# Performance work log

Hardware: AMD Instinct MI355X
Metric: run time of the kernel (lower is better)

## Reference

```python
import jax, jax.numpy as jnp
import numpy as np

D_MODEL = 1024
NUM_HEADS = 16
D_K = D_MODEL // NUM_HEADS


def setup_inputs() -> dict:
    key = jax.random.key(0)
    k_x, k_q, k_k, k_v, k_o = jax.random.split(key, 5)
    s = 1.0 / np.sqrt(D_MODEL)
    return {
        "x": jax.random.normal(k_x, (2, 2048, D_MODEL), dtype=jnp.float32),
        "W_q": jax.random.normal(k_q, (D_MODEL, D_MODEL), dtype=jnp.float32) * s,
        "W_k": jax.random.normal(k_k, (D_MODEL, D_MODEL), dtype=jnp.float32) * s,
        "W_v": jax.random.normal(k_v, (D_MODEL, D_MODEL), dtype=jnp.float32) * s,
        "W_o": jax.random.normal(k_o, (D_MODEL, D_MODEL), dtype=jnp.float32) * s,
    }


def reference(x, W_q, W_k, W_v, W_o):
    B, S, D = x.shape
    H, dk = NUM_HEADS, D_K
    # nn.Linear(y) = y @ W.T ; weights stored as (out, in)
    def proj(W):
        return (x @ W.T).reshape(B, S, H, dk).transpose(0, 2, 1, 3)  # (B,H,S,dk)
    Q, K, V = proj(W_q), proj(W_k), proj(W_v)
    scores = jnp.einsum("bhqd,bhkd->bhqk", Q, K) / np.sqrt(dk)  # (B,H,S,S)
    attn = jax.nn.softmax(scores, axis=-1)
    out = jnp.einsum("bhqk,bhkd->bhqd", attn, V)  # (B,H,S,dk)
    out = out.transpose(0, 2, 1, 3).reshape(B, S, D)
    return out @ W_o.T
```

## Files before the change

### kernel.cpp

```cpp
#include <hip/hip_runtime.h>
#include <hip/hip_bf16.h>

#define SEQ 2048
#define DM  1024
#define NH  16
#define DK  64
#define MROWS 4096

typedef __attribute__((ext_vector_type(8))) short short8;
typedef __attribute__((ext_vector_type(4))) short short4v;
typedef __attribute__((ext_vector_type(4))) float float4v;
typedef __attribute__((ext_vector_type(2))) unsigned uint2v;

typedef const __attribute__((address_space(1))) unsigned gu32;
typedef __attribute__((address_space(3))) unsigned lu32;

__device__ __forceinline__ void gl2lds16(const void* g, void* l) {
  __builtin_amdgcn_global_load_lds((gu32*)g, (lu32*)l, 16, 0, 0);
}

__device__ __forceinline__ short f2bf(float f) {
  union { float f; unsigned u; } v; v.f = f;
  unsigned r = v.u + 0x7fffu + ((v.u >> 16) & 1u);
  return (short)(r >> 16);
}

#if __has_builtin(__builtin_amdgcn_exp2f)
#define EXP2(x) __builtin_amdgcn_exp2f(x)
#else
#define EXP2(x) exp2f(x)
#endif

__device__ __forceinline__ unsigned pack_bfu(float a, float b) {
  unsigned ua = __float_as_uint(a) + 0x8000u;
  unsigned ub = __float_as_uint(b) + 0x8000u;
#if __has_builtin(__builtin_amdgcn_perm)
  return __builtin_amdgcn_perm(ub, ua, 0x07060302u);
#else
  return (ua >> 16) | (ub & 0xffff0000u);
#endif
}

__global__ __launch_bounds__(256) void cvt_kernel(
    const float* __restrict__ in, short* __restrict__ out) {
  int i = blockIdx.x * 256 + threadIdx.x;
  float4v f = ((const float4v*)in)[i];
  short4v s;
#pragma unroll
  for (int j = 0; j < 4; ++j) s[j] = f2bf(f[j]);
  ((short4v*)out)[i] = s;
}

__global__ __launch_bounds__(256) void cvt4_kernel(
    const float* __restrict__ a, const float* __restrict__ b,
    const float* __restrict__ c, const float* __restrict__ d,
    short* __restrict__ out) {
  const float* srcs[4] = {a, b, c, d};
  const float* s = srcs[blockIdx.y];
  int i = blockIdx.x * 256 + threadIdx.x;
  float4v f = ((const float4v*)s)[i];
  short4v sv;
#pragma unroll
  for (int j = 0; j < 4; ++j) sv[j] = f2bf(f[j]);
  ((short4v*)(out + (size_t)blockIdx.y * DM * DM))[i] = sv;
}

template<int WMW, int WNW, int WNSZ, typename TC>
__global__ __launch_bounds__(WMW*WNW*64, 3) void gemm_bt(
    const short* __restrict__ A, const short* __restrict__ Bw0,
    TC* __restrict__ C0, int M, int N, int K, size_t strB, size_t strC,
    short* __restrict__ vtOut, float qs0)
{
  constexpr int WAVES = WMW * WNW, THREADS = WAVES * 64;
  constexpr int TM = WMW * 64, TN = WNW * WNSZ, NI = WNSZ / 16;
  constexpr int CA = TM * 64 / (8 * THREADS);
  constexpr int CB = TN * 64 / (8 * THREADS);
  constexpr int SM_SZ = (WMW == 2 && WNW == 2) ? 128 * 136 : (TM + TN) * 64;
  __shared__ __align__(16) short SMEM[SM_SZ];
  short* Al = SMEM;
  short* Bl = SMEM + TM * 64;

  const short* Bw = Bw0 + (size_t)blockIdx.z * strB;
  TC* C = C0 + (size_t)blockIdx.z * strC;

  const int tid  = threadIdx.x;
  const int lane = tid & 63, wave = tid >> 6;
  const int l16  = lane & 15, quad = lane >> 4;
  const int wm   = (wave / WNW) * 64, wn = (wave % WNW) * WNSZ;
  const int cm   = blockIdx.y * TM, cn = blockIdx.x * TN;

  float4v acc[4][NI];
#pragma unroll
  for (int i = 0; i < 4; ++i)
#pragma unroll
    for (int j = 0; j < NI; ++j)
#pragma unroll
      for (int r = 0; r < 4; ++r) acc[i][j][r] = 0.f;

  const short* ag = A  + (size_t)cm * K;
  const short* bg = Bw + (size_t)cn * K;

  auto stage = [&](int k0) {
#pragma unroll
    for (int i = 0; i < CA; ++i) {
      int c = i * THREADS + tid;
      int row = c >> 3, cg = (c & 7) ^ (row & 7);
      gl2lds16(ag + (size_t)row * K + k0 + cg * 8,
               &Al[(i * WAVES + wave) * 512]);
    }
#pragma unroll
    for (int i = 0; i < CB; ++i) {
      int c = i * THREADS + tid;
      int row = c >> 3, cg = (c & 7) ^ (row & 7);
      gl2lds16(bg + (size_t)row * K + k0 + cg * 8,
               &Bl[(i * WAVES + wave) * 512]);
    }
  };
  auto compute = [&]() {
#pragma unroll
    for (int ks = 0; ks < 2; ++ks) {
      const int sw = ((ks * 4 + quad) ^ (l16 & 7)) << 3;
      short8 af[4], bfr[NI];
#pragma unroll
      for (int mi = 0; mi < 4; ++mi)
        af[mi] = *(const short8*)&Al[(wm + mi*16 + l16) * 64 + sw];
#pragma unroll
      for (int ni = 0; ni < NI; ++ni)
        bfr[ni] = *(const short8*)&Bl[(wn + ni*16 + l16) * 64 + sw];
#pragma unroll
      for (int mi = 0; mi < 4; ++mi)
#pragma unroll
        for (int ni = 0; ni < NI; ++ni)
          acc[mi][ni] = __builtin_amdgcn_mfma_f32_16x16x32_bf16(
              af[mi], bfr[ni], acc[mi][ni], 0, 0, 0);
    }
  };

  for (int k0 = 0; k0 < K; k0 += 64) {
    stage(k0);
    __syncthreads();
    compute();
    __syncthreads();
  }

  const float scl = (blockIdx.z == 0) ? qs0 : 1.f;

  if constexpr (WMW == 2 && WNW == 2) {
    if (vtOut != nullptr && blockIdx.z == 2) {
      short* T = SMEM;
#pragma unroll
      for (int mi = 0; mi < 4; ++mi)
#pragma unroll
        for (int ni = 0; ni < 4; ++ni)
#pragma unroll
          for (int r = 0; r < 4; ++r)
            T[(wn + ni*16 + l16) * 136 + wm + mi*16 + quad*4 + r] =
                f2bf(acc[mi][ni][r]);
      __syncthreads();
      const int nrow = tid >> 1, mo = (tid & 1) * 64;
      const int b = cm >> 11;
      const int s0 = (cm & (SEQ - 1)) + mo;
      short* vt = vtOut + ((size_t)b * DM + cn + nrow) * SEQ + s0;
#pragma unroll
      for (int j = 0; j < 8; ++j)
        *(short8*)(vt + j * 8) = *(const short8*)&T[nrow * 136 + mo + j * 8];
      return;
    }
  }
#pragma unroll
  for (int mi = 0; mi < 4; ++mi)
#pragma unroll
    for (int ni = 0; ni < NI; ++ni)
#pragma unroll
      for (int r = 0; r < 4; ++r) {
        int m = cm + wm + mi*16 + quad*4 + r;
        int n = cn + wn + ni*16 + l16;
        float v = acc[mi][ni][r] * scl;
        if constexpr (sizeof(TC) == 2) C[(size_t)m * N + n] = f2bf(v);
        else                           C[(size_t)m * N + n] = v;
      }
}

__global__ __launch_bounds__(256, 3) void flash_kernel(
    const short* __restrict__ Q, const short* __restrict__ Kg,
    const short* __restrict__ VTg, short* __restrict__ AO)
{
  __shared__ __align__(16) short Kl[2][64 * 64];
  __shared__ __align__(16) short Vt[2][64 * 64];
  __shared__ __align__(16) short Pl[4][32 * 64];
  __shared__ float lsumL[4][32];
  const int tid  = threadIdx.x;
  const int lane = tid & 63, wave = tid >> 6;
  const int l16  = lane & 15, quad = lane >> 4;
  const int hc   = blockIdx.x * DK;
  const int q0   = blockIdx.y * 128;
  const size_t base = (size_t)blockIdx.z * SEQ;

  short8 qfr[2][2];
#pragma unroll
  for (int qf = 0; qf < 2; ++qf)
#pragma unroll
    for (int ks = 0; ks < 2; ++ks)
      qfr[qf][ks] = *(const short8*)(Q + (base + q0 + wave*32 + qf*16 + l16) * DM
                                     + hc + ks*32 + quad*8);

  float4v O[2][4];
  float lsum[2] = {0.f, 0.f};
#pragma unroll
  for (int mt = 0; mt < 2; ++mt)
#pragma unroll
    for (int nt = 0; nt < 4; ++nt)
#pragma unroll
      for (int r = 0; r < 4; ++r) O[mt][nt][r] = 0.f;

  const float4v z4 = {0.f, 0.f, 0.f, 0.f};
  const short* vtb = VTg + ((size_t)blockIdx.z * DM + hc) * SEQ;

  auto stageKV = [&](int buf, int kb) {
#pragma unroll
    for (int i = 0; i < 2; ++i) {
      int c = i * 256 + tid;
      int row = c >> 3, cg = (c & 7) ^ (row & 7);
      gl2lds16(Kg + (base + kb*64 + row) * DM + hc + cg * 8,
               &Kl[buf][(i * 4 + wave) * 512]);
      gl2lds16(vtb + (size_t)row * SEQ + kb*64 + cg * 8,
               &Vt[buf][(i * 4 + wave) * 512]);
    }
  };

  stageKV(0, 0);
  __syncthreads();

  int cur = 0;
  for (int kb = 0; kb < SEQ / 64; ++kb) {
    bool nxt = (kb + 1 < SEQ / 64);
    if (nxt) stageKV(cur ^ 1, kb + 1);

    float4v s[4][2];
#pragma unroll
    for (int kf = 0; kf < 4; ++kf) {
      const int rowb = (kf*16 + l16) * 64;
      short8 k0 = *(const short8*)&Kl[cur][rowb + ((quad       ^ (l16 & 7)) << 3)];
      short8 k1 = *(const short8*)&Kl[cur][rowb + (((4 + quad) ^ (l16 & 7)) << 3)];
#pragma unroll
      for (int qf = 0; qf < 2; ++qf) {
        float4v t = __builtin_amdgcn_mfma_f32_16x16x32_bf16(k0, qfr[qf][0], z4, 0, 0, 0);
        s[kf][qf]  = __builtin_amdgcn_mfma_f32_16x16x32_bf16(k1, qfr[qf][1], t, 0, 0, 0);
      }
    }
#pragma unroll
    for (int kf = 0; kf < 4; ++kf)
#pragma unroll
      for (int qf = 0; qf < 2; ++qf) {
        float p0 = EXP2(s[kf][qf][0]), p1 = EXP2(s[kf][qf][1]);
        float p2 = EXP2(s[kf][qf][2]), p3 = EXP2(s[kf][qf][3]);
        lsum[qf] += (p0 + p1) + (p2 + p3);
        uint2v pk;
        pk[0] = pack_bfu(p0, p1);
        pk[1] = pack_bfu(p2, p3);
        *(uint2v*)&Pl[wave][(qf*16 + l16) * 64 +
                            ((kf*16 + quad*4) ^ ((l16 & 7) << 3))] = pk;
      }
#pragma unroll
    for (int ks = 0; ks < 2; ++ks) {
      const int sw = ((ks*4 + quad) ^ (l16 & 7)) << 3;
      short8 pf[2];
#pragma unroll
      for (int mt = 0; mt < 2; ++mt)
        pf[mt] = *(const short8*)&Pl[wave][(mt*16 + l16) * 64 + sw];
#pragma unroll
      for (int nt = 0; nt < 4; ++nt) {
        short8 vf = *(const short8*)&Vt[cur][(nt*16 + l16) * 64 + sw];
#pragma unroll
        for (int mt = 0; mt < 2; ++mt)
          O[mt][nt] = __builtin_amdgcn_mfma_f32_16x16x32_bf16(
              pf[mt], vf, O[mt][nt], 0, 0, 0);
      }
    }
    __syncthreads();
    cur ^= 1;
  }

#pragma unroll
  for (int qf = 0; qf < 2; ++qf) {
    float l = lsum[qf];
    l += __shfl_xor(l, 16, 64);
    l += __shfl_xor(l, 32, 64);
    lsumL[wave][qf*16 + l16] = l;
  }
#pragma unroll
  for (int mt = 0; mt < 2; ++mt) {
    float inv[4];
#pragma unroll
    for (int r = 0; r < 4; ++r)
      inv[r] = 1.f / lsumL[wave][mt*16 + quad*4 + r];
#pragma unroll
    for (int nt = 0; nt < 4; ++nt)
#pragma unroll
      for (int r = 0; r < 4; ++r) {
        int m = q0 + wave*32 + mt*16 + quad*4 + r;
        AO[(base + m) * DM + hc + nt*16 + l16] = f2bf(O[mt][nt][r] * inv[r]);
      }
  }
}

extern "C" void kernel_launch(void* const* d_in, const int* in_sizes, int n_in,
                              void* d_out, int out_size, void* d_ws, size_t ws_size,
                              hipStream_t stream) {
  (void)in_sizes; (void)n_in; (void)out_size; (void)ws_size;
  const float* x  = (const float*)d_in[0];
  const float* Wq = (const float*)d_in[1];
  const float* Wk = (const float*)d_in[2];
  const float* Wv = (const float*)d_in[3];
  const float* Wo = (const float*)d_in[4];
  float* out = (float*)d_out;

  const size_t NX = (size_t)MROWS * DM;
  const size_t NW = (size_t)DM * DM;
  short* xb  = (short*)d_ws;
  short* Wqb = xb  + NX;
  short* Qb  = Wqb + 4 * NW;
  short* Kb  = Qb  + NX;
  short* AO  = Kb  + NX;
  short* VTb = AO  + NX;

  cvt_kernel<<<dim3(NX / 4 / 256), 256, 0, stream>>>(x, xb);
  cvt4_kernel<<<dim3(NW / 4 / 256, 4), 256, 0, stream>>>(Wq, Wk, Wv, Wo, Wqb);

  const float qs = 0.18033688011112042f;

  gemm_bt<2, 2, 64, short><<<dim3(DM / 128, MROWS / 128, 3), 256, 0, stream>>>(
      xb, Wqb, Qb, MROWS, DM, DM, NW, NX, VTb, qs);

  flash_kernel<<<dim3(NH, SEQ / 128, 2), 256, 0, stream>>>(Qb, Kb, VTb, AO);

  gemm_bt<1, 4, 32, float><<<dim3(DM / 128, MROWS / 64, 1), 256, 0, stream>>>(
      AO, Wqb + 3 * NW, out, MROWS, DM, DM, 0, 0, nullptr, 1.f);
}
```

Measured before the change: 181.8 us.

## Double-buffer GEMM LDS staging with BK=32 and a single barrier per step

The bf16 GEMM's K loop now uses BK=32 with two LDS buffers. The next slice is prefetched through global_load_lds while MFMAs run on the current one, and each step needs one barrier instead of two. The LDS swizzle is reworked for 32-wide rows, and the output GEMM's min-waves launch bound is lowered to 2. This aims to hide global load latency at the cost of more loop iterations, with fewer MFMAs per barrier.

```diff
diff --git a/kernel.cpp b/kernel.cpp
--- a/kernel.cpp
+++ b/kernel.cpp
@@ -65,20 +65,20 @@
   ((short4v*)(out + (size_t)blockIdx.y * DM * DM))[i] = sv;
 }
 
-template<int WMW, int WNW, int WNSZ, typename TC>
-__global__ __launch_bounds__(WMW*WNW*64, 3) void gemm_bt(
+template<int WMW, int WNW, int WNSZ, int MINW, typename TC>
+__global__ __launch_bounds__(WMW*WNW*64, MINW) void gemm_bt(
     const short* __restrict__ A, const short* __restrict__ Bw0,
     TC* __restrict__ C0, int M, int N, int K, size_t strB, size_t strC,
     short* __restrict__ vtOut, float qs0)
 {
   constexpr int WAVES = WMW * WNW, THREADS = WAVES * 64;
   constexpr int TM = WMW * 64, TN = WNW * WNSZ, NI = WNSZ / 16;
-  constexpr int CA = TM * 64 / (8 * THREADS);
-  constexpr int CB = TN * 64 / (8 * THREADS);
-  constexpr int SM_SZ = (WMW == 2 && WNW == 2) ? 128 * 136 : (TM + TN) * 64;
+  constexpr int CA = TM * 32 / (8 * THREADS);
+  constexpr int CB = TN * 32 / (8 * THREADS);
+  constexpr int STG = 2 * (TM + TN) * 32;
+  constexpr int SM_SZ = (WMW == 2 && WNW == 2) ?
+      (STG > 128 * 136 ? STG : 128 * 136) : STG;
   __shared__ __align__(16) short SMEM[SM_SZ];
-  short* Al = SMEM;
-  short* Bl = SMEM + TM * 64;
 
   const short* Bw = Bw0 + (size_t)blockIdx.z * strB;
   TC* C = C0 + (size_t)blockIdx.z * strC;
@@ -100,47 +100,52 @@
   const short* ag = A  + (size_t)cm * K;
   const short* bg = Bw + (size_t)cn * K;
 
-  auto stage = [&](int k0) {
+  auto stage = [&](int buf, int k0) {
 #pragma unroll
     for (int i = 0; i < CA; ++i) {
-      int c = i * THREADS + tid;
-      int row = c >> 3, cg = (c & 7) ^ (row & 7);
-      gl2lds16(ag + (size_t)row * K + k0 + cg * 8,
-               &Al[(i * WAVES + wave) * 512]);
+      int s = i * THREADS + tid;
+      int row = s >> 2, cgl = (s & 3) ^ ((row >> 1) & 3);
+      gl2lds16(ag + (size_t)row * K + k0 + cgl * 8,
+               &SMEM[buf * TM * 32 + (i * WAVES + wave) * 512]);
     }
 #pragma unroll
     for (int i = 0; i < CB; ++i) {
-      int c = i * THREADS + tid;
-      int row = c >> 3, cg = (c & 7) ^ (row & 7);
-      gl2lds16(bg + (size_t)row * K + k0 + cg * 8,
-               &Bl[(i * WAVES + wave) * 512]);
+      int s = i * THREADS + tid;
+      int row = s >> 2, cgl = (s & 3) ^ ((row >> 1) & 3);
+      gl2lds16(bg + (size_t)row * K + k0 + cgl * 8,
+               &SMEM[2 * TM * 32 + buf * TN * 32 + (i * WAVES + wave) * 512]);
     }
   };
-  auto compute = [&]() {
-#pragma unroll
-    for (int ks = 0; ks < 2; ++ks) {
-      const int sw = ((ks * 4 + quad) ^ (l16 & 7)) << 3;
-      short8 af[4], bfr[NI];
-#pragma unroll
-      for (int mi = 0; mi < 4; ++mi)
-        af[mi] = *(const short8*)&Al[(wm + mi*16 + l16) * 64 + sw];
+  auto compute = [&](int buf) {
+    const short* Al = &SMEM[buf * TM * 32];
+    const short* Bl = &SMEM[2 * TM * 32 + buf * TN * 32];
+    short8 af[4], bfr[NI];
+#pragma unroll
+    for (int mi = 0; mi < 4; ++mi) {
+      int row = wm + mi*16 + l16;
+      af[mi] = *(const short8*)&Al[row * 32 + ((quad ^ ((row >> 1) & 3)) << 3)];
+    }
+#pragma unroll
+    for (int ni = 0; ni < NI; ++ni) {
+      int row = wn + ni*16 + l16;
+      bfr[ni] = *(const short8*)&Bl[row * 32 + ((quad ^ ((row >> 1) & 3)) << 3)];
+    }
+#pragma unroll
+    for (int mi = 0; mi < 4; ++mi)
 #pragma unroll
       for (int ni = 0; ni < NI; ++ni)
-        bfr[ni] = *(const short8*)&Bl[(wn + ni*16 + l16) * 64 + sw];
-#pragma unroll
-      for (int mi = 0; mi < 4; ++mi)
-#pragma unroll
-        for (int ni = 0; ni < NI; ++ni)
-          acc[mi][ni] = __builtin_amdgcn_mfma_f32_16x16x32_bf16(
-              af[mi], bfr[ni], acc[mi][ni], 0, 0, 0);
-    }
+        acc[mi][ni] = __builtin_amdgcn_mfma_f32_16x16x32_bf16(
+            af[mi], bfr[ni], acc[mi][ni], 0, 0, 0);
   };
 
-  for (int k0 = 0; k0 < K; k0 += 64) {
-    stage(k0);
+  stage(0, 0);
+  __syncthreads();
+  int cur = 0;
+  for (int k0 = 0; k0 < K; k0 += 32) {
+    if (k0 + 32 < K) stage(cur ^ 1, k0 + 32);
+    compute(cur);
     __syncthreads();
-    compute();
-    __syncthreads();
+    cur ^= 1;
   }
 
   const float scl = (blockIdx.z == 0) ? qs0 : 1.f;
@@ -329,11 +334,11 @@
 
   const float qs = 0.18033688011112042f;
 
-  gemm_bt<2, 2, 64, short><<<dim3(DM / 128, MROWS / 128, 3), 256, 0, stream>>>(
+  gemm_bt<2, 2, 64, 3, short><<<dim3(DM / 128, MROWS / 128, 3), 256, 0, stream>>>(
       xb, Wqb, Qb, MROWS, DM, DM, NW, NX, VTb, qs);
 
   flash_kernel<<<dim3(NH, SEQ / 128, 2), 256, 0, stream>>>(Qb, Kb, VTb, AO);
 
-  gemm_bt<1, 4, 32, float><<<dim3(DM / 128, MROWS / 64, 1), 256, 0, stream>>>(
+  gemm_bt<1, 4, 32, 2, float><<<dim3(DM / 128, MROWS / 64, 1), 256, 0, stream>>>(
       AO, Wqb + 3 * NW, out, MROWS, DM, DM, 0, 0, nullptr, 1.f);
 }
```

After: 186.8 us. 2.8% more time.

## Shrink GEMM tiles and double flash waves per block for higher occupancy

Applied to the files above, without the earlier changes.

The GEMM kernel is re-templated on tile sizes: QKV projection uses 64x128 tiles and output projection 64x64 tiles, each with 2x2 waves holding 32-row fragments, with min-blocks raised to 6. The flash attention kernel now uses 8 waves of 16 query rows each instead of 4 waves of 32 rows, so each thread stages one K/V chunk and keeps fewer accumulators. The intent is to cut register pressure and launch more waves to hide latency. In exchange each tile gets less reuse per LDS load, and more global traffic is spent re-fetching A and B tiles.

```diff
diff --git a/kernel.cpp b/kernel.cpp
--- a/kernel.cpp
+++ b/kernel.cpp
@@ -65,17 +65,18 @@
   ((short4v*)(out + (size_t)blockIdx.y * DM * DM))[i] = sv;
 }
 
-template<int WMW, int WNW, int WNSZ, typename TC>
-__global__ __launch_bounds__(WMW*WNW*64, 3) void gemm_bt(
+template<int TM, int TN, int MINW, typename TC>
+__global__ __launch_bounds__(256, MINW) void gemm_bt(
     const short* __restrict__ A, const short* __restrict__ Bw0,
     TC* __restrict__ C0, int M, int N, int K, size_t strB, size_t strC,
     short* __restrict__ vtOut, float qs0)
 {
-  constexpr int WAVES = WMW * WNW, THREADS = WAVES * 64;
-  constexpr int TM = WMW * 64, TN = WNW * WNSZ, NI = WNSZ / 16;
-  constexpr int CA = TM * 64 / (8 * THREADS);
-  constexpr int CB = TN * 64 / (8 * THREADS);
-  constexpr int SM_SZ = (WMW == 2 && WNW == 2) ? 128 * 136 : (TM + TN) * 64;
+  constexpr int NI = TN / 32;
+  constexpr int CA = TM * 64 / (8 * 256);
+  constexpr int CB = TN * 64 / (8 * 256);
+  constexpr int STG = (TM + TN) * 64;
+  constexpr int TSZ = TN * 72;
+  constexpr int SM_SZ = (TN == 128 && TSZ > STG) ? TSZ : STG;
   __shared__ __align__(16) short SMEM[SM_SZ];
   short* Al = SMEM;
   short* Bl = SMEM + TM * 64;
@@ -86,12 +87,12 @@
   const int tid  = threadIdx.x;
   const int lane = tid & 63, wave = tid >> 6;
   const int l16  = lane & 15, quad = lane >> 4;
-  const int wm   = (wave / WNW) * 64, wn = (wave % WNW) * WNSZ;
+  const int wm   = (wave >> 1) * 32, wn = (wave & 1) * (TN / 2);
   const int cm   = blockIdx.y * TM, cn = blockIdx.x * TN;
 
-  float4v acc[4][NI];
-#pragma unroll
-  for (int i = 0; i < 4; ++i)
+  float4v acc[2][NI];
+#pragma unroll
+  for (int i = 0; i < 2; ++i)
 #pragma unroll
     for (int j = 0; j < NI; ++j)
 #pragma unroll
@@ -103,32 +104,30 @@
   auto stage = [&](int k0) {
 #pragma unroll
     for (int i = 0; i < CA; ++i) {
-      int c = i * THREADS + tid;
+      int c = i * 256 + tid;
       int row = c >> 3, cg = (c & 7) ^ (row & 7);
-      gl2lds16(ag + (size_t)row * K + k0 + cg * 8,
-               &Al[(i * WAVES + wave) * 512]);
+      gl2lds16(ag + (size_t)row * K + k0 + cg * 8, &Al[(i * 4 + wave) * 512]);
     }
 #pragma unroll
     for (int i = 0; i < CB; ++i) {
-      int c = i * THREADS + tid;
+      int c = i * 256 + tid;
       int row = c >> 3, cg = (c & 7) ^ (row & 7);
-      gl2lds16(bg + (size_t)row * K + k0 + cg * 8,
-               &Bl[(i * WAVES + wave) * 512]);
+      gl2lds16(bg + (size_t)row * K + k0 + cg * 8, &Bl[(i * 4 + wave) * 512]);
     }
   };
   auto compute = [&]() {
 #pragma unroll
     for (int ks = 0; ks < 2; ++ks) {
       const int sw = ((ks * 4 + quad) ^ (l16 & 7)) << 3;
-      short8 af[4], bfr[NI];
-#pragma unroll
-      for (int mi = 0; mi < 4; ++mi)
+      short8 af[2], bfr[NI];
+#pragma unroll
+      for (int mi = 0; mi < 2; ++mi)
         af[mi] = *(const short8*)&Al[(wm + mi*16 + l16) * 64 + sw];
 #pragma unroll
       for (int ni = 0; ni < NI; ++ni)
         bfr[ni] = *(const short8*)&Bl[(wn + ni*16 + l16) * 64 + sw];
 #pragma unroll
-      for (int mi = 0; mi < 4; ++mi)
+      for (int mi = 0; mi < 2; ++mi)
 #pragma unroll
         for (int ni = 0; ni < NI; ++ni)
           acc[mi][ni] = __builtin_amdgcn_mfma_f32_16x16x32_bf16(
@@ -145,30 +144,30 @@
 
   const float scl = (blockIdx.z == 0) ? qs0 : 1.f;
 
-  if constexpr (WMW == 2 && WNW == 2) {
+  if constexpr (TN == 128) {
     if (vtOut != nullptr && blockIdx.z == 2) {
       short* T = SMEM;
 #pragma unroll
-      for (int mi = 0; mi < 4; ++mi)
-#pragma unroll
-        for (int ni = 0; ni < 4; ++ni)
+      for (int mi = 0; mi < 2; ++mi)
+#pragma unroll
+        for (int ni = 0; ni < NI; ++ni)
 #pragma unroll
           for (int r = 0; r < 4; ++r)
-            T[(wn + ni*16 + l16) * 136 + wm + mi*16 + quad*4 + r] =
+            T[(wn + ni*16 + l16) * 72 + wm + mi*16 + quad*4 + r] =
                 f2bf(acc[mi][ni][r]);
       __syncthreads();
-      const int nrow = tid >> 1, mo = (tid & 1) * 64;
+      const int nrow = tid >> 1, mo = (tid & 1) * 32;
       const int b = cm >> 11;
       const int s0 = (cm & (SEQ - 1)) + mo;
       short* vt = vtOut + ((size_t)b * DM + cn + nrow) * SEQ + s0;
 #pragma unroll
-      for (int j = 0; j < 8; ++j)
-        *(short8*)(vt + j * 8) = *(const short8*)&T[nrow * 136 + mo + j * 8];
+      for (int j = 0; j < 4; ++j)
+        *(short8*)(vt + j * 8) = *(const short8*)&T[nrow * 72 + mo + j * 8];
       return;
     }
   }
 #pragma unroll
-  for (int mi = 0; mi < 4; ++mi)
+  for (int mi = 0; mi < 2; ++mi)
 #pragma unroll
     for (int ni = 0; ni < NI; ++ni)
 #pragma unroll
@@ -181,14 +180,14 @@
       }
 }
 
-__global__ __launch_bounds__(256, 3) void flash_kernel(
+__global__ __launch_bounds__(512, 4) void flash_kernel(
     const short* __restrict__ Q, const short* __restrict__ Kg,
     const short* __restrict__ VTg, short* __restrict__ AO)
 {
   __shared__ __align__(16) short Kl[2][64 * 64];
   __shared__ __align__(16) short Vt[2][64 * 64];
-  __shared__ __align__(16) short Pl[4][32 * 64];
-  __shared__ float lsumL[4][32];
+  __shared__ __align__(16) short Pl[8][16 * 64];
+  __shared__ float lsumL[8][16];
   const int tid  = threadIdx.x;
   const int lane = tid & 63, wave = tid >> 6;
   const int l16  = lane & 15, quad = lane >> 4;
@@ -196,36 +195,26 @@
   const int q0   = blockIdx.y * 128;
   const size_t base = (size_t)blockIdx.z * SEQ;
 
-  short8 qfr[2][2];
-#pragma unroll
-  for (int qf = 0; qf < 2; ++qf)
-#pragma unroll
-    for (int ks = 0; ks < 2; ++ks)
-      qfr[qf][ks] = *(const short8*)(Q + (base + q0 + wave*32 + qf*16 + l16) * DM
-                                     + hc + ks*32 + quad*8);
-
-  float4v O[2][4];
-  float lsum[2] = {0.f, 0.f};
-#pragma unroll
-  for (int mt = 0; mt < 2; ++mt)
-#pragma unroll
-    for (int nt = 0; nt < 4; ++nt)
-#pragma unroll
-      for (int r = 0; r < 4; ++r) O[mt][nt][r] = 0.f;
+  short8 qfr[2];
+#pragma unroll
+  for (int ks = 0; ks < 2; ++ks)
+    qfr[ks] = *(const short8*)(Q + (base + q0 + wave*16 + l16) * DM
+                               + hc + ks*32 + quad*8);
+
+  float4v O[4];
+  float lsum = 0.f;
+#pragma unroll
+  for (int nt = 0; nt < 4; ++nt)
+#pragma unroll
+    for (int r = 0; r < 4; ++r) O[nt][r] = 0.f;
 
   const float4v z4 = {0.f, 0.f, 0.f, 0.f};
   const short* vtb = VTg + ((size_t)blockIdx.z * DM + hc) * SEQ;
 
   auto stageKV = [&](int buf, int kb) {
-#pragma unroll
-    for (int i = 0; i < 2; ++i) {
-      int c = i * 256 + tid;
-      int row = c >> 3, cg = (c & 7) ^ (row & 7);
-      gl2lds16(Kg + (base + kb*64 + row) * DM + hc + cg * 8,
-               &Kl[buf][(i * 4 + wave) * 512]);
-      gl2lds16(vtb + (size_t)row * SEQ + kb*64 + cg * 8,
-               &Vt[buf][(i * 4 + wave) * 512]);
-    }
+    int row = tid >> 3, cg = (tid & 7) ^ (row & 7);
+    gl2lds16(Kg + (base + kb*64 + row) * DM + hc + cg * 8, &Kl[buf][wave * 512]);
+    gl2lds16(vtb + (size_t)row * SEQ + kb*64 + cg * 8, &Vt[buf][wave * 512]);
   };
 
   stageKV(0, 0);
@@ -233,75 +222,58 @@
 
   int cur = 0;
   for (int kb = 0; kb < SEQ / 64; ++kb) {
-    bool nxt = (kb + 1 < SEQ / 64);
-    if (nxt) stageKV(cur ^ 1, kb + 1);
-
-    float4v s[4][2];
+    if (kb + 1 < SEQ / 64) stageKV(cur ^ 1, kb + 1);
+
+    float4v s[4];
 #pragma unroll
     for (int kf = 0; kf < 4; ++kf) {
       const int rowb = (kf*16 + l16) * 64;
       short8 k0 = *(const short8*)&Kl[cur][rowb + ((quad       ^ (l16 & 7)) << 3)];
       short8 k1 = *(const short8*)&Kl[cur][rowb + (((4 + quad) ^ (l16 & 7)) << 3)];
-#pragma unroll
-      for (int qf = 0; qf < 2; ++qf) {
-        float4v t = __builtin_amdgcn_mfma_f32_16x16x32_bf16(k0, qfr[qf][0], z4, 0, 0, 0);
-        s[kf][qf]  = __builtin_amdgcn_mfma_f32_16x16x32_bf16(k1, qfr[qf][1], t, 0, 0, 0);
-      }
-    }
-#pragma unroll
-    for (int kf = 0; kf < 4; ++kf)
-#pragma unroll
-      for (int qf = 0; qf < 2; ++qf) {
-        float p0 = EXP2(s[kf][qf][0]), p1 = EXP2(s[kf][qf][1]);
-        float p2 = EXP2(s[kf][qf][2]), p3 = EXP2(s[kf][qf][3]);
-        lsum[qf] += (p0 + p1) + (p2 + p3);
-        uint2v pk;
-        pk[0] = pack_bfu(p0, p1);
-        pk[1] = pack_bfu(p2, p3);
-        *(uint2v*)&Pl[wave][(qf*16 + l16) * 64 +
-                            ((kf*16 + quad*4) ^ ((l16 & 7) << 3))] = pk;
-      }
+      float4v t = __builtin_amdgcn_mfma_f32_16x16x32_bf16(k0, qfr[0], z4, 0, 0, 0);
+      s[kf]     = __builtin_amdgcn_mfma_f32_16x16x32_bf16(k1, qfr[1], t, 0, 0, 0);
+    }
+#pragma unroll
+    for (int kf = 0; kf < 4; ++kf) {
+      float p0 = EXP2(s[kf][0]), p1 = EXP2(s[kf][1]);
+      float p2 = EXP2(s[kf][2]), p3 = EXP2(s[kf][3]);
+      lsum += (p0 + p1) + (p2 + p3);
+      uint2v pk;
+      pk[0] = pack_bfu(p0, p1);
+      pk[1] = pack_bfu(p2, p3);
+      *(uint2v*)&Pl[wave][l16 * 64 +
+                          ((kf*16 + quad*4) ^ ((l16 & 7) << 3))] = pk;
+    }
 #pragma unroll
     for (int ks = 0; ks < 2; ++ks) {
       const int sw = ((ks*4 + quad) ^ (l16 & 7)) << 3;
-      short8 pf[2];
-#pragma unroll
-      for (int mt = 0; mt < 2; ++mt)
-        pf[mt] = *(const short8*)&Pl[wave][(mt*16 + l16) * 64 + sw];
+      short8 pf = *(const short8*)&Pl[wave][l16 * 64 + sw];
 #pragma unroll
       for (int nt = 0; nt < 4; ++nt) {
         short8 vf = *(const short8*)&Vt[cur][(nt*16 + l16) * 64 + sw];
-#pragma unroll
-        for (int mt = 0; mt < 2; ++mt)
-          O[mt][nt] = __builtin_amdgcn_mfma_f32_16x16x32_bf16(
-              pf[mt], vf, O[mt][nt], 0, 0, 0);
+        O[nt] = __builtin_amdgcn_mfma_f32_16x16x32_bf16(pf, vf, O[nt], 0, 0, 0);
       }
     }
     __syncthreads();
     cur ^= 1;
   }
 
-#pragma unroll
-  for (int qf = 0; qf < 2; ++qf) {
-    float l = lsum[qf];
+  {
+    float l = lsum;
     l += __shfl_xor(l, 16, 64);
     l += __shfl_xor(l, 32, 64);
-    lsumL[wave][qf*16 + l16] = l;
+    lsumL[wave][l16] = l;
   }
-#pragma unroll
-  for (int mt = 0; mt < 2; ++mt) {
-    float inv[4];
-#pragma unroll
-    for (int r = 0; r < 4; ++r)
-      inv[r] = 1.f / lsumL[wave][mt*16 + quad*4 + r];
-#pragma unroll
-    for (int nt = 0; nt < 4; ++nt)
-#pragma unroll
-      for (int r = 0; r < 4; ++r) {
-        int m = q0 + wave*32 + mt*16 + quad*4 + r;
-        AO[(base + m) * DM + hc + nt*16 + l16] = f2bf(O[mt][nt][r] * inv[r]);
-      }
-  }
+  float inv[4];
+#pragma unroll
+  for (int r = 0; r < 4; ++r) inv[r] = 1.f / lsumL[wave][quad*4 + r];
+#pragma unroll
+  for (int nt = 0; nt < 4; ++nt)
+#pragma unroll
+    for (int r = 0; r < 4; ++r) {
+      int m = q0 + wave*16 + quad*4 + r;
+      AO[(base + m) * DM + hc + nt*16 + l16] = f2bf(O[nt][r] * inv[r]);
+    }
 }
 
 extern "C" void kernel_launch(void* const* d_in, const int* in_sizes, int n_in,
@@ -329,11 +301,11 @@
 
   const float qs = 0.18033688011112042f;
 
-  gemm_bt<2, 2, 64, short><<<dim3(DM / 128, MROWS / 128, 3), 256, 0, stream>>>(
+  gemm_bt<64, 128, 6, short><<<dim3(DM / 128, MROWS / 64, 3), 256, 0, stream>>>(
       xb, Wqb, Qb, MROWS, DM, DM, NW, NX, VTb, qs);
 
-  flash_kernel<<<dim3(NH, SEQ / 128, 2), 256, 0, stream>>>(Qb, Kb, VTb, AO);
-
-  gemm_bt<1, 4, 32, float><<<dim3(DM / 128, MROWS / 64, 1), 256, 0, stream>>>(
+  flash_kernel<<<dim3(NH, SEQ / 128, 2), 512, 0, stream>>>(Qb, Kb, VTb, AO);
+
+  gemm_bt<64, 64, 6, float><<<dim3(DM / 64, MROWS / 64, 1), 256, 0, stream>>>(
       AO, Wqb + 3 * NW, out, MROWS, DM, DM, 0, 0, nullptr, 1.f);
 }
```

Result: slower. 187.6 us (+3.2%).
